# Performance work log

Hardware: AMD Instinct MI355X
Metric: run time of the kernel (lower is better)

The kernel has to match this reference:

```python
import jax, jax.numpy as jnp
import numpy as np

BS, SEQ, DIN, HID, H = 2, 2048, 1024, 1024, 16
D = HID // H  # head_size = 64

def setup_inputs() -> dict:
    key = jax.random.key(0)
    ks = jax.random.split(key, 9)
    s = 0.02
    return {
        "x":    jax.random.normal(ks[0], (BS, SEQ, DIN), jnp.float32),
        "Wq":   jax.random.normal(ks[1], (DIN, HID), jnp.float32) * s,
        "bq":   jax.random.normal(ks[2], (HID,), jnp.float32) * s,
        "Wk":   jax.random.normal(ks[3], (DIN, HID), jnp.float32) * s,
        "bk":   jax.random.normal(ks[4], (HID,), jnp.float32) * s,
        "Wv":   jax.random.normal(ks[5], (DIN, HID), jnp.float32) * s,
        "bv":   jax.random.normal(ks[6], (HID,), jnp.float32) * s,
        "Wmix": jax.random.normal(ks[7], (HID, HID), jnp.float32) * s,
        "bmix": jax.random.normal(ks[8], (HID,), jnp.float32) * s,
    }

def reference(x, Wq, bq, Wk, bk, Wv, bv, Wmix, bmix):
    bs, seq, _ = x.shape
    scale = jnp.asarray(D ** 0.5, x.dtype)
    # projections, split heads: [b, s, H, D] (contiguous channel slices per head,
    # equivalent to the torch transpose/reshape dance)
    q = (x @ Wq + bq).reshape(bs, seq, H, D)
    k = (x @ Wk + bk).reshape(bs, seq, H, D)
    v = (x @ Wv + bv).reshape(bs, seq, H, D)
    scores = jnp.einsum('bqhd,bkhd->bhqk', q, k) / scale  # [b, H, seq, seq]
    causal_mask = jnp.triu(jnp.ones((seq, seq), bool), k=1)
    scores = jnp.where(causal_mask, -jnp.inf, scores)
    probs = jax.nn.softmax(scores, axis=-1)
    att = jnp.einsum('bhqk,bkhd->bqhd', probs, v).reshape(bs, seq, HID)
    return att @ Wmix + bmix
```

## Files before the change

### kernel.cpp

```cpp
#include <hip/hip_runtime.h>
#include <hip/hip_bf16.h>

#define BS 2
#define SEQ 2048
#define DIN 1024
#define HID 1024
#define NH 16
#define HD 64
#define M_ROWS (BS*SEQ)
#define NQKV 3072

typedef __attribute__((ext_vector_type(8))) short short8;
typedef __attribute__((ext_vector_type(4))) short short4v;
typedef __attribute__((ext_vector_type(8))) __bf16 bf16x8;
typedef __attribute__((ext_vector_type(4))) float floatx4;

__device__ __forceinline__ short f2bf(float f) {
  return __builtin_bit_cast(short, (__bf16)f);
}
__device__ __forceinline__ float bf2f(short s) {
  return __uint_as_float(((unsigned)(unsigned short)s) << 16);
}

__device__ __forceinline__ floatx4 mfma16(short8 a, short8 b, floatx4 c) {
  return __builtin_amdgcn_mfma_f32_16x16x32_bf16(
      __builtin_bit_cast(bf16x8, a), __builtin_bit_cast(bf16x8, b), c, 0, 0, 0);
}

__device__ __forceinline__ float exp2fast(float x) {
#if __has_builtin(__builtin_amdgcn_exp2f)
  return __builtin_amdgcn_exp2f(x);
#else
  return exp2f(x);
#endif
}

__device__ __forceinline__ void gload_lds16(const void* g, void* l) {
  __builtin_amdgcn_global_load_lds(
      (const __attribute__((address_space(1))) unsigned int*)g,
      (__attribute__((address_space(3))) unsigned int*)l, 16, 0, 0);
}

__device__ __forceinline__ int swz_off(int row, int colsh) {
  return row * 128 + ((colsh * 2) ^ ((row & 7) << 4));
}

__global__ __launch_bounds__(256) void prep_kernel(
    const float* __restrict__ x,
    const float* __restrict__ Wq, const float* __restrict__ Wk,
    const float* __restrict__ Wv, const float* __restrict__ Wmix,
    short* __restrict__ xb, short* __restrict__ Wt, short* __restrict__ Wmixt)
{
  __shared__ float Ws[64][65];
  if (blockIdx.z < 4) {
    const float* src; short* dst;
    switch (blockIdx.z) {
      case 0:  src = Wq;   dst = Wt;                 break;
      case 1:  src = Wk;   dst = Wt + (1u << 20);    break;
      case 2:  src = Wv;   dst = Wt + (2u << 20);    break;
      default: src = Wmix; dst = Wmixt;              break;
    }
    const int n0 = blockIdx.x * 64, k0 = blockIdx.y * 64;
    const int c = threadIdx.x & 63, r0 = threadIdx.x >> 6;
    #pragma unroll
    for (int i = 0; i < 16; ++i) {
      int rr = r0 + 4 * i;
      Ws[rr][c] = src[(size_t)(k0 + rr) * DIN + n0 + c];
    }
    __syncthreads();
    #pragma unroll
    for (int i = 0; i < 16; ++i) {
      int cc = r0 + 4 * i;
      dst[(size_t)(n0 + cc) * DIN + k0 + c] = f2bf(Ws[c][cc]);
    }
  } else {
    const int bb = blockIdx.y * 16 + blockIdx.x;
    const int gid0 = bb * 256 + threadIdx.x;
    const float4* x4 = (const float4*)x;
    #pragma unroll
    for (int it = 0; it < 8; ++it) {
      int gid = gid0 + it * 65536;
      float4 v0 = x4[2 * gid], v1 = x4[2 * gid + 1];
      short8 o;
      o[0] = f2bf(v0.x); o[1] = f2bf(v0.y); o[2] = f2bf(v0.z); o[3] = f2bf(v0.w);
      o[4] = f2bf(v1.x); o[5] = f2bf(v1.y); o[6] = f2bf(v1.z); o[7] = f2bf(v1.w);
      *(short8*)&xb[(size_t)gid * 8] = o;
    }
  }
}

template<int BM, int BN, bool OUT_F32, bool QKV>
__global__ __launch_bounds__(256) void gemm_kernel(
    const short* __restrict__ A, const short* __restrict__ Bt,
    const float* __restrict__ bias0, const float* __restrict__ bias1,
    const float* __restrict__ bias2, void* __restrict__ Cp,
    short* __restrict__ vt, int Ndim, int Kdim)
{
  constexpr int MT = BM / 32, NT = BN / 32;
  __shared__ short As[BM * 64];
  __shared__ short Bs[BN * 64];
  const int tid = threadIdx.x;
  const int wid = tid >> 6, lane = tid & 63, lg = lane >> 4, lm = lane & 15;
  const int wr = wid >> 1, wc = wid & 1;

  const int nwgx = gridDim.x;
  const int nwg = nwgx * gridDim.y;
  const int idlin = blockIdx.y * nwgx + blockIdx.x;
  const int sw = (idlin & 7) * (nwg >> 3) + (idlin >> 3);
  const int m0 = (sw / nwgx) * BM, n0 = (sw % nwgx) * BN;

  floatx4 acc[MT][NT];
  #pragma unroll
  for (int i = 0; i < MT; ++i)
    #pragma unroll
    for (int j = 0; j < NT; ++j) acc[i][j] = floatx4{0.f, 0.f, 0.f, 0.f};

  for (int k0 = 0; k0 < Kdim; k0 += 64) {
    __syncthreads();
    #pragma unroll
    for (int j = 0; j < BM / 32; ++j) {
      int flat = tid + 256 * j;
      int row = flat >> 3, ch = (flat & 7) ^ (row & 7);
      gload_lds16(A + (size_t)(m0 + row) * Kdim + k0 + ch * 8,
                  (char*)As + wid * 1024 + j * 4096);
    }
    #pragma unroll
    for (int j = 0; j < BN / 32; ++j) {
      int flat = tid + 256 * j;
      int row = flat >> 3, ch = (flat & 7) ^ (row & 7);
      gload_lds16(Bt + (size_t)(n0 + row) * Kdim + k0 + ch * 8,
                  (char*)Bs + wid * 1024 + j * 4096);
    }
    __syncthreads();

    #pragma unroll
    for (int kk = 0; kk < 2; ++kk) {
      short8 a[MT], b[NT];
      #pragma unroll
      for (int mt = 0; mt < MT; ++mt) {
        int row = wr * (BM / 2) + mt * 16 + lm;
        int ch = (kk * 4 + lg) ^ (row & 7);
        a[mt] = *(const short8*)&As[row * 64 + ch * 8];
      }
      #pragma unroll
      for (int nt = 0; nt < NT; ++nt) {
        int row = wc * (BN / 2) + nt * 16 + lm;
        int ch = (kk * 4 + lg) ^ (row & 7);
        b[nt] = *(const short8*)&Bs[row * 64 + ch * 8];
      }
      #pragma unroll
      for (int mt = 0; mt < MT; ++mt)
        #pragma unroll
        for (int nt = 0; nt < NT; ++nt)
          acc[mt][nt] = mfma16(a[mt], b[nt], acc[mt][nt]);
    }
  }

  #pragma unroll
  for (int mt = 0; mt < MT; ++mt) {
    const int row0 = m0 + wr * (BM / 2) + mt * 16 + 4 * lg;
    #pragma unroll
    for (int nt = 0; nt < NT; ++nt) {
      const int col = n0 + wc * (BN / 2) + nt * 16 + lm;
      const float* bp = bias0;
      if (QKV) bp = (col < 1024) ? bias0 : (col < 2048 ? bias1 : bias2);
      const float bv = bp[col & 1023];
      if (QKV && n0 >= 2048) {
        int hd = col - 2048;
        int bb = row0 >> 11, s = row0 & 2047;
        short4v pv;
        #pragma unroll
        for (int r = 0; r < 4; ++r) pv[r] = f2bf(acc[mt][nt][r] + bv);
        *(short4v*)&vt[((size_t)(bb * (NH * HD) + hd)) * SEQ + s] = pv;
      } else {
        #pragma unroll
        for (int r = 0; r < 4; ++r) {
          float v = acc[mt][nt][r] + bv;
          if (OUT_F32) ((float*)Cp)[(size_t)(row0 + r) * Ndim + col] = v;
          else         ((short*)Cp)[(size_t)(row0 + r) * Ndim + col] = f2bf(v);
        }
      }
    }
  }
}

#define MFIX 12.0f
__global__ __launch_bounds__(256, 4) void attn_kernel(
    const short* __restrict__ qkv, const short* __restrict__ vt,
    short* __restrict__ att, short* __restrict__ pO, float* __restrict__ pml)
{
  __shared__ short Ks[2 * 64 * 64];
  __shared__ short Vs[2 * 64 * 64];
  __shared__ short Ps[4 * 16 * 64];
  const int tid = threadIdx.x;
  const int wid = tid >> 6, lane = tid & 63, lg = lane >> 4, lm = lane & 15;

  int id = blockIdx.x, x, c;
  if (id < 4)        { x = id;                       c = 0;        }
  else if (id < 12)  { int t = id - 4;   x = 4  + (t >> 1); c = t & 1; }
  else if (id < 24)  { int t = id - 12;  x = 8  + t / 3;    c = t % 3; }
  else if (id < 40)  { int t = id - 24;  x = 12 + (t >> 2); c = t & 3; }
  else if (id < 60)  { int t = id - 40;  x = 16 + t / 5;    c = t % 5; }
  else if (id < 84)  { int t = id - 60;  x = 20 + t / 6;    c = t % 6; }
  else if (id < 112) { int t = id - 84;  x = 24 + t / 7;    c = t % 7; }
  else               { int t = id - 112; x = 28 + (t >> 3); c = t & 7; }
  const int nch = (x >> 2) + 1;
  const int tb = c * 4;
  const int te = min(tb + 4, x + 1);
  const int q0 = x * 64;
  const int bh = blockIdx.y, b = bh >> 4, h = bh & 15;
  const short* qp = qkv + (size_t)(b * SEQ) * NQKV + h * HD;
  const short* kp = qp + HID;
  const short* vp = vt + (size_t)bh * HD * SEQ;

  const float cl2 = 0.18033688011112042f;
  const int qrow_g = q0 + wid * 16 + lm;
  short8 qf[2];
  {
    const short* qrow = qp + (size_t)qrow_g * NQKV;
    #pragma unroll
    for (int kk = 0; kk < 2; ++kk) {
      short8 raw = *(const short8*)(qrow + kk * 32 + lg * 8);
      #pragma unroll
      for (int j = 0; j < 8; ++j) qf[kk][j] = f2bf(bf2f(raw[j]) * cl2);
    }
  }

  short8 ones;
  #pragma unroll
  for (int j = 0; j < 8; ++j) ones[j] = (short)0x3F80;

  const int rstage = tid >> 3, c8 = (tid & 7) * 8;
  int soff[2], koff[2][4], pw[4], pr[2];
  #pragma unroll
  for (int i = 0; i < 2; ++i) soff[i] = swz_off(rstage + 32 * i, c8);
  #pragma unroll
  for (int kk = 0; kk < 2; ++kk)
    #pragma unroll
    for (int nt = 0; nt < 4; ++nt)
      koff[kk][nt] = swz_off(nt * 16 + lm, kk * 32 + lg * 8);
  #pragma unroll
  for (int nt = 0; nt < 4; ++nt) pw[nt] = swz_off(lm, nt * 16 + 4 * lg);
  #pragma unroll
  for (int kk = 0; kk < 2; ++kk) pr[kk] = swz_off(lm, kk * 32 + lg * 8);

  const short* kgp[2];
  const short* vgp[2];
  short8 kreg[2], vreg[2];
  #pragma unroll
  for (int i = 0; i < 2; ++i) {
    kgp[i] = kp + (size_t)(tb * 64 + rstage + 32 * i) * NQKV + c8;
    vgp[i] = vp + (size_t)(rstage + 32 * i) * SEQ + tb * 64 + c8;
    kreg[i] = *(const short8*)kgp[i];
    vreg[i] = *(const short8*)vgp[i];
  }

  char* psw = (char*)(Ps + wid * 16 * 64);
  floatx4 o[4];
  floatx4 ol = floatx4{0.f, 0.f, 0.f, 0.f};
  #pragma unroll
  for (int nt = 0; nt < 4; ++nt) o[nt] = floatx4{0.f, 0.f, 0.f, 0.f};

  for (int t = tb; t < te; ++t) {
    const int cb = (t - tb) & 1;
    char* Kb = (char*)Ks + cb * 8192;
    char* Vb = (char*)Vs + cb * 8192;
    #pragma unroll
    for (int i = 0; i < 2; ++i) {
      *(short8*)(Kb + soff[i]) = kreg[i];
      *(short8*)(Vb + soff[i]) = vreg[i];
    }
    if (t + 1 < te) {
      #pragma unroll
      for (int i = 0; i < 2; ++i) {
        kgp[i] += 64 * NQKV;
        vgp[i] += 64;
        kreg[i] = *(const short8*)kgp[i];
        vreg[i] = *(const short8*)vgp[i];
      }
    }
    __syncthreads();

    floatx4 s[4];
    #pragma unroll
    for (int nt = 0; nt < 4; ++nt) s[nt] = floatx4{-MFIX, -MFIX, -MFIX, -MFIX};
    __builtin_amdgcn_s_setprio(1);
    #pragma unroll
    for (int kk = 0; kk < 2; ++kk)
      #pragma unroll
      for (int nt = 0; nt < 4; ++nt)
        s[nt] = mfma16(*(const short8*)(Kb + koff[kk][nt]), qf[kk], s[nt]);
    __builtin_amdgcn_s_setprio(0);

    if (t == x) {
      #pragma unroll
      for (int nt = 0; nt < 4; ++nt)
        #pragma unroll
        for (int r = 0; r < 4; ++r) {
          int kv = t * 64 + nt * 16 + 4 * lg + r;
          if (kv > qrow_g) s[nt][r] = -3e38f;
        }
    }

    #pragma unroll
    for (int nt = 0; nt < 4; ++nt) {
      short4v pv;
      #pragma unroll
      for (int r = 0; r < 4; ++r) pv[r] = f2bf(exp2fast(s[nt][r]));
      *(short4v*)(psw + pw[nt]) = pv;
    }

    #pragma unroll
    for (int kk = 0; kk < 2; ++kk) {
      short8 pf = *(const short8*)(psw + pr[kk]);
      __builtin_amdgcn_s_setprio(1);
      #pragma unroll
      for (int nt = 0; nt < 4; ++nt)
        o[nt] = mfma16(*(const short8*)(Vb + koff[kk][nt]), pf, o[nt]);
      ol = mfma16(ones, pf, ol);
      __builtin_amdgcn_s_setprio(0);
    }
  }

  if (nch == 1) {
    const float linv = 1.0f / ol[0];
    #pragma unroll
    for (int nt = 0; nt < 4; ++nt) {
      short4v ov;
      #pragma unroll
      for (int r = 0; r < 4; ++r) ov[r] = f2bf(o[nt][r] * linv);
      *(short4v*)&att[((size_t)(b * SEQ + qrow_g)) * HID + h * HD + nt * 16 + 4 * lg] = ov;
    }
  } else {
    const int g = x >> 2;
    const int slot = bh * 140 + (2 * g * g + 2 * g - 4 + (x & 3) * (g + 1)) + c;
    short* po = pO + (size_t)slot * 4096;
    const int ql = wid * 16 + lm;
    #pragma unroll
    for (int nt = 0; nt < 4; ++nt) {
      short4v ov;
      #pragma unroll
      for (int r = 0; r < 4; ++r) ov[r] = f2bf(o[nt][r]);
      *(short4v*)&po[ql * 64 + nt * 16 + 4 * lg] = ov;
    }
    if (lane < 16) {
      pml[slot * 128 + 64 + ql] = ol[0];
    }
  }
}

__global__ __launch_bounds__(256) void combine_kernel(
    const short* __restrict__ pO, const float* __restrict__ pml,
    short* __restrict__ att)
{
  const int x = 4 + blockIdx.x;
  const int bh = blockIdx.y, b = bh >> 4, h = bh & 15;
  const int g = x >> 2;
  const int nch = g + 1;
  const int tid = threadIdx.x;
  const int row = tid >> 2, d0 = (tid & 3) * 16;
  const int base_slot = bh * 140 + (2 * g * g + 2 * g - 4 + (x & 3) * (g + 1));

  float L = 0.f;
  for (int cc = 0; cc < nch; ++cc)
    L += pml[(base_slot + cc) * 128 + 64 + row];
  const float inv = 1.0f / L;

  float acc[16];
  #pragma unroll
  for (int j = 0; j < 16; ++j) acc[j] = 0.f;
  for (int cc = 0; cc < nch; ++cc) {
    const short* po = pO + (size_t)(base_slot + cc) * 4096 + row * 64 + d0;
    short8 v0 = *(const short8*)po, v1 = *(const short8*)(po + 8);
    #pragma unroll
    for (int j = 0; j < 8; ++j) {
      acc[j]     += bf2f(v0[j]);
      acc[j + 8] += bf2f(v1[j]);
    }
  }
  short8 o0, o1;
  #pragma unroll
  for (int j = 0; j < 8; ++j) {
    o0[j] = f2bf(acc[j] * inv);
    o1[j] = f2bf(acc[j + 8] * inv);
  }
  short* dst = att + ((size_t)(b * SEQ + x * 64 + row)) * HID + h * HD + d0;
  *(short8*)dst = o0;
  *(short8*)(dst + 8) = o1;
}

extern "C" void kernel_launch(void* const* d_in, const int* in_sizes, int n_in,
                              void* d_out, int out_size, void* d_ws, size_t ws_size,
                              hipStream_t stream) {
  (void)in_sizes; (void)n_in; (void)out_size; (void)ws_size;
  const float* x    = (const float*)d_in[0];
  const float* Wq   = (const float*)d_in[1];
  const float* bq   = (const float*)d_in[2];
  const float* Wk   = (const float*)d_in[3];
  const float* bk   = (const float*)d_in[4];
  const float* Wv   = (const float*)d_in[5];
  const float* bv   = (const float*)d_in[6];
  const float* Wmix = (const float*)d_in[7];
  const float* bmix = (const float*)d_in[8];
  float* out = (float*)d_out;

  char* w = (char*)d_ws;
  short* xb      = (short*)w; w += (size_t)8 << 20;
  short* Wt      = (short*)w; w += (size_t)6 << 20;
  short* Wmixt   = (short*)w; w += (size_t)2 << 20;
  short* qkvb    = (short*)w; w += (size_t)24 << 20;
  short* vtb     = (short*)w; w += (size_t)8 << 20;
  short* ab      = (short*)w; w += (size_t)8 << 20;
  short* pO      = (short*)w; w += (size_t)140 * 32 * 4096 * 2;
  float* pml     = (float*)w;

  hipLaunchKernelGGL(prep_kernel, dim3(16, 16, 5), dim3(256), 0, stream,
                     x, Wq, Wk, Wv, Wmix, xb, Wt, Wmixt);

  hipLaunchKernelGGL((gemm_kernel<128, 128, false, true>), dim3(NQKV / 128, M_ROWS / 128),
                     dim3(256), 0, stream, xb, Wt, bq, bk, bv, (void*)qkvb, vtb, NQKV, DIN);

  hipLaunchKernelGGL(attn_kernel, dim3(144, BS * NH), dim3(256), 0, stream,
                     qkvb, vtb, ab, pO, pml);
  hipLaunchKernelGGL(combine_kernel, dim3(28, BS * NH), dim3(256), 0, stream,
                     pO, pml, ab);

  hipLaunchKernelGGL((gemm_kernel<64, 128, true, false>), dim3(HID / 128, M_ROWS / 64),
                     dim3(256), 0, stream, ab, Wmixt, bmix, bmix, bmix, (void*)out,
                     (short*)nullptr, HID, DIN);
}
```

Before: 105.0 us.

## Switch attention to 32x32x16 MFMA with split-K warp layout and LDS reduction

Reworks the attention kernel so each wave computes a 32x32 score tile with the 32x32x16 bf16 MFMA. The four waves split into two query halves times two key halves, and partial O and row sums are reduced through shared memory at the end. The row sum now comes from scalar accumulation of the exponentials instead of an extra MFMA against a ones vector. This adds more LDS for P and the reduction, an extra synchronised reduction pass, and more registers, and occupancy is lowered to 3 blocks per SM.

Measured after the change: 122.3 us. 1.16x slower.

```diff
diff --git a/kernel.cpp b/kernel.cpp
--- a/kernel.cpp
+++ b/kernel.cpp
@@ -14,6 +14,7 @@
 typedef __attribute__((ext_vector_type(4))) short short4v;
 typedef __attribute__((ext_vector_type(8))) __bf16 bf16x8;
 typedef __attribute__((ext_vector_type(4))) float floatx4;
+typedef __attribute__((ext_vector_type(16))) float floatx16;
 
 __device__ __forceinline__ short f2bf(float f) {
   return __builtin_bit_cast(short, (__bf16)f);
@@ -24,6 +25,10 @@
 
 __device__ __forceinline__ floatx4 mfma16(short8 a, short8 b, floatx4 c) {
   return __builtin_amdgcn_mfma_f32_16x16x32_bf16(
+      __builtin_bit_cast(bf16x8, a), __builtin_bit_cast(bf16x8, b), c, 0, 0, 0);
+}
+__device__ __forceinline__ floatx16 mfma32(short8 a, short8 b, floatx16 c) {
+  return __builtin_amdgcn_mfma_f32_32x32x16_bf16(
       __builtin_bit_cast(bf16x8, a), __builtin_bit_cast(bf16x8, b), c, 0, 0, 0);
 }
 
@@ -185,15 +190,18 @@
 }
 
 #define MFIX 12.0f
-__global__ __launch_bounds__(256, 4) void attn_kernel(
+__global__ __launch_bounds__(256, 3) void attn_kernel(
     const short* __restrict__ qkv, const short* __restrict__ vt,
     short* __restrict__ att, short* __restrict__ pO, float* __restrict__ pml)
 {
   __shared__ short Ks[2 * 64 * 64];
   __shared__ short Vs[2 * 64 * 64];
-  __shared__ short Ps[4 * 16 * 64];
+  __shared__ short Ps[4 * 32 * 64];
+  __shared__ float Lb[2][32];
   const int tid = threadIdx.x;
-  const int wid = tid >> 6, lane = tid & 63, lg = lane >> 4, lm = lane & 15;
+  const int wid = tid >> 6, lane = tid & 63;
+  const int l32 = lane & 31, lh = lane >> 5;
+  const int wq = wid & 1, wk = wid >> 1;
 
   int id = blockIdx.x, x, c;
   if (id < 4)        { x = id;                       c = 0;        }
@@ -214,35 +222,33 @@
   const short* vp = vt + (size_t)bh * HD * SEQ;
 
   const float cl2 = 0.18033688011112042f;
-  const int qrow_g = q0 + wid * 16 + lm;
-  short8 qf[2];
+  const int qrow_g = q0 + wq * 32 + l32;
+  short8 qf[4];
   {
     const short* qrow = qp + (size_t)qrow_g * NQKV;
     #pragma unroll
-    for (int kk = 0; kk < 2; ++kk) {
-      short8 raw = *(const short8*)(qrow + kk * 32 + lg * 8);
-      #pragma unroll
-      for (int j = 0; j < 8; ++j) qf[kk][j] = f2bf(bf2f(raw[j]) * cl2);
-    }
-  }
-
-  short8 ones;
-  #pragma unroll
-  for (int j = 0; j < 8; ++j) ones[j] = (short)0x3F80;
+    for (int kb = 0; kb < 4; ++kb) {
+      short8 raw = *(const short8*)(qrow + kb * 16 + lh * 8);
+      #pragma unroll
+      for (int j = 0; j < 8; ++j) qf[kb][j] = f2bf(bf2f(raw[j]) * cl2);
+    }
+  }
 
   const int rstage = tid >> 3, c8 = (tid & 7) * 8;
-  int soff[2], koff[2][4], pw[4], pr[2];
+  int soff[2], koff[4], voff[2][2], pwo[4], pro[2];
   #pragma unroll
   for (int i = 0; i < 2; ++i) soff[i] = swz_off(rstage + 32 * i, c8);
   #pragma unroll
-  for (int kk = 0; kk < 2; ++kk)
-    #pragma unroll
-    for (int nt = 0; nt < 4; ++nt)
-      koff[kk][nt] = swz_off(nt * 16 + lm, kk * 32 + lg * 8);
-  #pragma unroll
-  for (int nt = 0; nt < 4; ++nt) pw[nt] = swz_off(lm, nt * 16 + 4 * lg);
-  #pragma unroll
-  for (int kk = 0; kk < 2; ++kk) pr[kk] = swz_off(lm, kk * 32 + lg * 8);
+  for (int kb = 0; kb < 4; ++kb) koff[kb] = swz_off(wk * 32 + l32, kb * 16 + lh * 8);
+  #pragma unroll
+  for (int ks = 0; ks < 2; ++ks)
+    #pragma unroll
+    for (int db = 0; db < 2; ++db)
+      voff[ks][db] = swz_off(db * 32 + l32, wk * 32 + ks * 16 + lh * 8);
+  #pragma unroll
+  for (int i = 0; i < 4; ++i) pwo[i] = swz_off(l32, 8 * i + 4 * lh);
+  #pragma unroll
+  for (int ks = 0; ks < 2; ++ks) pro[ks] = swz_off(l32, ks * 16 + 8 * lh);
 
   const short* kgp[2];
   const short* vgp[2];
@@ -255,11 +261,11 @@
     vreg[i] = *(const short8*)vgp[i];
   }
 
-  char* psw = (char*)(Ps + wid * 16 * 64);
-  floatx4 o[4];
-  floatx4 ol = floatx4{0.f, 0.f, 0.f, 0.f};
-  #pragma unroll
-  for (int nt = 0; nt < 4; ++nt) o[nt] = floatx4{0.f, 0.f, 0.f, 0.f};
+  char* psw = (char*)(Ps + wid * 32 * 64);
+  floatx16 o0, o1;
+  #pragma unroll
+  for (int j = 0; j < 16; ++j) { o0[j] = 0.f; o1[j] = 0.f; }
+  float lpart = 0.f;
 
   for (int t = tb; t < te; ++t) {
     const int cb = (t - tb) & 1;
@@ -281,70 +287,105 @@
     }
     __syncthreads();
 
-    floatx4 s[4];
-    #pragma unroll
-    for (int nt = 0; nt < 4; ++nt) s[nt] = floatx4{-MFIX, -MFIX, -MFIX, -MFIX};
+    floatx16 s;
+    #pragma unroll
+    for (int j = 0; j < 16; ++j) s[j] = -MFIX;
     __builtin_amdgcn_s_setprio(1);
     #pragma unroll
-    for (int kk = 0; kk < 2; ++kk)
-      #pragma unroll
-      for (int nt = 0; nt < 4; ++nt)
-        s[nt] = mfma16(*(const short8*)(Kb + koff[kk][nt]), qf[kk], s[nt]);
+    for (int kb = 0; kb < 4; ++kb)
+      s = mfma32(*(const short8*)(Kb + koff[kb]), qf[kb], s);
     __builtin_amdgcn_s_setprio(0);
 
     if (t == x) {
       #pragma unroll
-      for (int nt = 0; nt < 4; ++nt)
+      for (int j = 0; j < 16; ++j) {
+        int kv = t * 64 + wk * 32 + (j & 3) + 8 * (j >> 2) + 4 * lh;
+        if (kv > qrow_g) s[j] = -3e38f;
+      }
+    }
+
+    #pragma unroll
+    for (int i = 0; i < 4; ++i) {
+      short4v pv;
+      #pragma unroll
+      for (int r = 0; r < 4; ++r) {
+        float e = exp2fast(s[4 * i + r]);
+        lpart += e;
+        pv[r] = f2bf(e);
+      }
+      *(short4v*)(psw + pwo[i]) = pv;
+    }
+
+    #pragma unroll
+    for (int ks = 0; ks < 2; ++ks) {
+      short8 pf = *(const short8*)(psw + pro[ks]);
+      __builtin_amdgcn_s_setprio(1);
+      o0 = mfma32(*(const short8*)(Vb + voff[ks][0]), pf, o0);
+      o1 = mfma32(*(const short8*)(Vb + voff[ks][1]), pf, o1);
+      __builtin_amdgcn_s_setprio(0);
+    }
+  }
+
+  lpart += __shfl_xor(lpart, 32);
+
+  __syncthreads();
+  float* Ob = (float*)Ps;
+  if (wk == 1) {
+    #pragma unroll
+    for (int db = 0; db < 2; ++db) {
+      #pragma unroll
+      for (int i = 0; i < 4; ++i) {
+        floatx4 v;
+        #pragma unroll
+        for (int r = 0; r < 4; ++r) v[r] = (db ? o1 : o0)[4 * i + r];
+        *(floatx4*)(Ob + wq * 2048 + l32 * 64 + db * 32 + 8 * i + 4 * lh) = v;
+      }
+    }
+    if (lh == 0) Lb[wq][l32] = lpart;
+  }
+  __syncthreads();
+  if (wk == 0) {
+    #pragma unroll
+    for (int db = 0; db < 2; ++db) {
+      #pragma unroll
+      for (int i = 0; i < 4; ++i) {
+        floatx4 v = *(const floatx4*)(Ob + wq * 2048 + l32 * 64 + db * 32 + 8 * i + 4 * lh);
         #pragma unroll
         for (int r = 0; r < 4; ++r) {
-          int kv = t * 64 + nt * 16 + 4 * lg + r;
-          if (kv > qrow_g) s[nt][r] = -3e38f;
+          if (db) o1[4 * i + r] += v[r];
+          else    o0[4 * i + r] += v[r];
         }
-    }
-
-    #pragma unroll
-    for (int nt = 0; nt < 4; ++nt) {
-      short4v pv;
-      #pragma unroll
-      for (int r = 0; r < 4; ++r) pv[r] = f2bf(exp2fast(s[nt][r]));
-      *(short4v*)(psw + pw[nt]) = pv;
-    }
-
-    #pragma unroll
-    for (int kk = 0; kk < 2; ++kk) {
-      short8 pf = *(const short8*)(psw + pr[kk]);
-      __builtin_amdgcn_s_setprio(1);
-      #pragma unroll
-      for (int nt = 0; nt < 4; ++nt)
-        o[nt] = mfma16(*(const short8*)(Vb + koff[kk][nt]), pf, o[nt]);
-      ol = mfma16(ones, pf, ol);
-      __builtin_amdgcn_s_setprio(0);
-    }
-  }
-
-  if (nch == 1) {
-    const float linv = 1.0f / ol[0];
-    #pragma unroll
-    for (int nt = 0; nt < 4; ++nt) {
-      short4v ov;
-      #pragma unroll
-      for (int r = 0; r < 4; ++r) ov[r] = f2bf(o[nt][r] * linv);
-      *(short4v*)&att[((size_t)(b * SEQ + qrow_g)) * HID + h * HD + nt * 16 + 4 * lg] = ov;
-    }
-  } else {
-    const int g = x >> 2;
-    const int slot = bh * 140 + (2 * g * g + 2 * g - 4 + (x & 3) * (g + 1)) + c;
-    short* po = pO + (size_t)slot * 4096;
-    const int ql = wid * 16 + lm;
-    #pragma unroll
-    for (int nt = 0; nt < 4; ++nt) {
-      short4v ov;
-      #pragma unroll
-      for (int r = 0; r < 4; ++r) ov[r] = f2bf(o[nt][r]);
-      *(short4v*)&po[ql * 64 + nt * 16 + 4 * lg] = ov;
-    }
-    if (lane < 16) {
-      pml[slot * 128 + 64 + ql] = ol[0];
+      }
+    }
+    lpart += Lb[wq][l32];
+
+    if (nch == 1) {
+      const float linv = 1.0f / lpart;
+      short* dst = att + ((size_t)(b * SEQ + qrow_g)) * HID + h * HD;
+      #pragma unroll
+      for (int db = 0; db < 2; ++db)
+        #pragma unroll
+        for (int i = 0; i < 4; ++i) {
+          short4v ov;
+          #pragma unroll
+          for (int r = 0; r < 4; ++r) ov[r] = f2bf((db ? o1 : o0)[4 * i + r] * linv);
+          *(short4v*)(dst + db * 32 + 8 * i + 4 * lh) = ov;
+        }
+    } else {
+      const int g = x >> 2;
+      const int slot = bh * 140 + (2 * g * g + 2 * g - 4 + (x & 3) * (g + 1)) + c;
+      short* po = pO + (size_t)slot * 4096;
+      const int ql = wq * 32 + l32;
+      #pragma unroll
+      for (int db = 0; db < 2; ++db)
+        #pragma unroll
+        for (int i = 0; i < 4; ++i) {
+          short4v ov;
+          #pragma unroll
+          for (int r = 0; r < 4; ++r) ov[r] = f2bf((db ? o1 : o0)[4 * i + r]);
+          *(short4v*)&po[ql * 64 + db * 32 + 8 * i + 4 * lh] = ov;
+        }
+      if (lh == 0) pml[slot * 128 + 64 + ql] = lpart;
     }
   }
 }
```
